# Kernel tuning notes

Measured on AMD Instinct MI355X. Metric: run time of the kernel, lower is better.

The kernel has to match this reference:

```python
import jax, jax.numpy as jnp
import numpy as np

B, S, D = 4, 4096, 64   # batch, seq_len, input_size
H, HD = 4, 16           # num_heads, head_dim


def setup_inputs() -> dict:
    key = jax.random.key(0)
    ks = jax.random.split(key, 9)
    sd = 1.0 / np.sqrt(D)          # torch Linear default uniform(-1/sqrt(fan_in), ...)
    so = 1.0 / np.sqrt(H * HD)
    u = lambda k, shape, s: jax.random.uniform(k, shape, jnp.float32, -s, s)
    return {
        "x": jax.random.normal(ks[0], (B, S, D), jnp.float32),
        "Wq": u(ks[1], (H, D, HD), sd), "bq": u(ks[2], (H, HD), sd),
        "Wk": u(ks[3], (H, D, HD), sd), "bk": u(ks[4], (H, HD), sd),
        "Wv": u(ks[5], (H, D, HD), sd), "bv": u(ks[6], (H, HD), sd),
        "Wo": u(ks[7], (H * HD, D), so), "bo": u(ks[8], (D,), so),
    }


def reference(x, Wq, bq, Wk, bk, Wv, bv, Wo, bo):
    # Batched per-head projections (fuses the original per-head Linear loop)
    q = jnp.einsum('bsd,hde->bhse', x, Wq) + bq[None, :, None, :]
    k = jnp.einsum('bsd,hde->bhse', x, Wk) + bk[None, :, None, :]
    v = jnp.einsum('bsd,hde->bhse', x, Wv) + bv[None, :, None, :]
    # scores: [B, H, S(query), S(key)]
    scores = jnp.einsum('bhse,bhte->bhst', q, k) / np.sqrt(HD).astype(np.float32)
    # FAITHFUL quirk: torch Softmax(dim=1) on [B,S,S] normalizes over the QUERY axis
    w = jax.nn.softmax(scores, axis=2)
    attended = jnp.einsum('bhst,bhte->bhse', w, v)          # [B,H,S,HD]
    concat = attended.transpose(0, 2, 1, 3).reshape(B, S, H * HD)
    out = concat @ Wo + bo                                   # [B,S,D]
    # FAITHFUL quirk: final softmax over the sequence axis (dim=1)
    return jax.nn.softmax(out, axis=1)
```

## Files before the change

kernel.cpp:

```cpp
#include <hip/hip_runtime.h>
#include <hip/hip_bf16.h>


#define BB 4
#define SS 4096
#define DD 64
#define HH 4
#define HDD 16

typedef unsigned int u32;
typedef unsigned short u16;
typedef __attribute__((ext_vector_type(8))) short bfrag;
typedef __attribute__((ext_vector_type(4))) float floatx4;
typedef __attribute__((ext_vector_type(16))) float floatx16;
typedef __attribute__((ext_vector_type(2))) u32 u32x2;
typedef __attribute__((ext_vector_type(4))) u32 u32x4;

#define LOG2E 1.4426950408889634074f
#define QSCALE (LOG2E * 0.25f)

__device__ __forceinline__ float fexp2(float x) {
#if __has_builtin(__builtin_amdgcn_exp2f)
  return __builtin_amdgcn_exp2f(x);
#else
  float r; asm("v_exp_f32 %0, %1" : "=v"(r) : "v"(x)); return r;
#endif
}
__device__ __forceinline__ float frcp(float x) {
#if __has_builtin(__builtin_amdgcn_rcpf)
  return __builtin_amdgcn_rcpf(x);
#else
  float r; asm("v_rcp_f32 %0, %1" : "=v"(r) : "v"(x)); return r;
#endif
}

__device__ __forceinline__ u16 f2bf(float f) {
  u32 u = __builtin_bit_cast(u32, f);
  return (u16)((u + 0x7FFFu + ((u >> 16) & 1u)) >> 16);
}
__device__ __forceinline__ u32 pack_bf(float lo, float hi) {
#if __has_builtin(__builtin_amdgcn_perm)
  return __builtin_amdgcn_perm(__builtin_bit_cast(u32, hi),
                               __builtin_bit_cast(u32, lo), 0x07060302u);
#else
  u32 a = __builtin_bit_cast(u32, lo);
  u32 b = __builtin_bit_cast(u32, hi);
  return (a >> 16) | (b & 0xFFFF0000u);
#endif
}

__device__ __forceinline__ void gload_lds16(const u16* g, u16* l) {
  __builtin_amdgcn_global_load_lds(
      (const __attribute__((address_space(1))) void*)(g),
      (__attribute__((address_space(3))) void*)(l), 16, 0, 0);
}

__device__ __forceinline__ int tmap(int c) {
  int c5 = c & 31;
  return (c & ~31) + (c5 & 3) + ((c5 >> 2) & 1) * 8 + ((c5 >> 3) & 1) * 16
       + ((c5 >> 4) & 1) * 4;
}

__global__ __launch_bounds__(256) void k_proj(
    const float* __restrict__ x,
    const float* __restrict__ Wq, const float* __restrict__ bq,
    const float* __restrict__ Wk, const float* __restrict__ bk,
    const float* __restrict__ Wv, const float* __restrict__ bv,
    u16* __restrict__ qb, u16* __restrict__ kb, float* __restrict__ vf)
{
  __shared__ float xs[16 * 64];
  const int tid = threadIdx.x;
  const int blk = blockIdx.x;
  const int b   = blk >> 8;
  const int s0  = (blk & 255) << 4;
  ((float4*)xs)[tid] = ((const float4*)(x + ((size_t)b * SS + s0) * DD))[tid];
  __syncthreads();

  const int col = tid & 63, h = col >> 4, e = col & 15;
  const int rg  = tid >> 6;
  float aq[4] = {0,0,0,0}, ak[4] = {0,0,0,0}, av[4] = {0,0,0,0};
  const int wofs = h * (DD * HDD) + e;
#pragma unroll 4
  for (int d = 0; d < DD; ++d) {
    float wq = Wq[wofs + d * HDD];
    float wk = Wk[wofs + d * HDD];
    float wv = Wv[wofs + d * HDD];
    const float* xr = xs + (rg * 4) * 64 + d;
#pragma unroll
    for (int r = 0; r < 4; ++r) {
      float xv = xr[r * 64];
      aq[r] += xv * wq; ak[r] += xv * wk; av[r] += xv * wv;
    }
  }
  const float bqv = bq[col], bkv = bk[col], bvv = bv[col];
  size_t base = ((size_t)(b * HH + h) * SS + (s0 + rg * 4)) * HDD + e;
#pragma unroll
  for (int r = 0; r < 4; ++r) {
    qb[base + r * HDD] = f2bf((aq[r] + bqv) * QSCALE);
    kb[base + r * HDD] = f2bf(ak[r] + bkv);
    vf[base + r * HDD] = av[r] + bvv;
  }
}

__global__ __launch_bounds__(512, 4) void k_csvp(
    const u16* __restrict__ qb, const u16* __restrict__ kb,
    const float* __restrict__ vf, u16* __restrict__ vp)
{
  __shared__ float vstage[128 * 16];
  __shared__ float cpart[2][128];
  __shared__ float rcl[128];
  const int tid = threadIdx.x;
  const int lane = tid & 63, w = tid >> 6;
  const int l31 = lane & 31, hl = lane >> 5;
  const int bx = blockIdx.x;
  const int bh = blockIdx.y;
  const int t0 = bx * 128 + (w & 3) * 32;
  const int shalf = w >> 2;
  const size_t base = (size_t)bh * (SS * HDD);

  {
    const float4* vsrc4 = (const float4*)(vf + ((size_t)bh * SS + bx * 128) * HDD);
    ((float4*)vstage)[tid] = vsrc4[tid];
  }

  const bfrag kf = *(const bfrag*)(kb + base + (size_t)(t0 + l31) * HDD + hl * 8);
  const u16* qpc = qb + base + ((size_t)shalf * 2048 + l31) * HDD + hl * 8;
  const floatx16 z16 = {0.f};
  float c0 = 0.f, c1 = 0.f, c2 = 0.f, c3 = 0.f;

#define LQ(i) (*(const bfrag*)(qpc + (size_t)(i) * (32 * HDD)))
#define ACCUM(dv)                                   \
  do {                                              \
    _Pragma("unroll")                               \
    for (int j = 0; j < 4; ++j) {                   \
      c0 += fexp2((dv)[4 * j + 0]);                 \
      c1 += fexp2((dv)[4 * j + 1]);                 \
      c2 += fexp2((dv)[4 * j + 2]);                 \
      c3 += fexp2((dv)[4 * j + 3]);                 \
    }                                               \
  } while (0)
#define STEP(qr, ri)                                                        \
  do {                                                                      \
    floatx16 dB = __builtin_amdgcn_mfma_f32_32x32x16_bf16(qr, kf, z16, 0, 0, 0); \
    qr = LQ(ri);                                                            \
    ACCUM(dA);                                                              \
    dA = dB;                                                                \
  } while (0)

  bfrag q0 = LQ(0), q1 = LQ(1), q2v = LQ(2), q3 = LQ(3);
  floatx16 dA = __builtin_amdgcn_mfma_f32_32x32x16_bf16(q0, kf, z16, 0, 0, 0);
  q0 = LQ(4);
#pragma unroll 1
  for (int o = 0; o < 2; ++o) {
#pragma unroll
    for (int i = 0; i < 32; i += 4) {
      STEP(q1,  i + 5);
      STEP(q2v, i + 6);
      STEP(q3,  i + 7);
      STEP(q0,  i + 8);
    }
    qpc += 32 * 32 * HDD;
  }
#undef STEP
#undef LQ
#undef ACCUM

  float c = (c0 + c1) + (c2 + c3);
  c += __shfl_xor(c, 32, 64);
  if (hl == 0)
    cpart[shalf][(w & 3) * 32 + l31] = c;
  __syncthreads();
  if (tid < 128)
    rcl[tid] = frcp(cpart[0][tid] + cpart[1][tid]);
  __syncthreads();

  if (tid < 256) {
    const int e = tid >> 4;
    const int h0 = bx & 1;
    const int poff = h0 * 16 + (tid & 15);
    const int cc = poff ^ (e & 7);
    const int h128 = h0 * 128;
    u32 r[4];
#pragma unroll
    for (int jj = 0; jj < 4; ++jj) {
      int ta = tmap(cc * 8 + 2 * jj)     - h128;
      int tb = tmap(cc * 8 + 2 * jj + 1) - h128;
      u16 lo = f2bf(vstage[ta * 16 + e] * rcl[ta]);
      u16 hi = f2bf(vstage[tb * 16 + e] * rcl[tb]);
      r[jj] = (u32)lo | ((u32)hi << 16);
    }
    u16* outb = vp + ((size_t)bh * 16 + (bx >> 1)) * 4096;
    u32x4 vv = {r[0], r[1], r[2], r[3]};
    *(u32x4*)(outb + e * 256 + poff * 8) = vv;
  }
}

__global__ __launch_bounds__(256, 4) void k_attn(
    const u16* __restrict__ qb, const u16* __restrict__ kb,
    const u16* __restrict__ vp, float* __restrict__ attp)
{
  __shared__ __align__(16) u16 vls[2][4096];
  const int tid  = threadIdx.x;
  const int lane = tid & 63, w = tid >> 6;
  const int l31 = lane & 31, hl = lane >> 5;
  const int bh = blockIdx.z, b = bh >> 2, h = bh & 3;
  const int tph = blockIdx.y;
  const int s0 = blockIdx.x * 128 + w * 32;
  const size_t base = (size_t)bh * (SS * HDD);

  const bfrag qf = *(const bfrag*)(qb + base + (size_t)(s0 + l31) * HDD + hl * 8);
  const u16* kp = kb + base + ((size_t)tph * 2048 + l31) * HDD + hl * 8;
  const floatx16 z16 = {0.f};
  floatx16 acc = {0.f};

  const u16* vsrc = vp + ((size_t)bh * 16 + tph * 8) * 4096;

  {
    const u16* gs = vsrc + w * 1024 + lane * 8;
    u16* ls = &vls[0][0] + w * 1024;
    gload_lds16(gs, ls);
    gload_lds16(gs + 512, ls + 512);
  }
  bfrag kfr[8];
#pragma unroll
  for (int it = 0; it < 8; ++it)
    kfr[it] = *(const bfrag*)(kp + (size_t)(it * 32) * HDD);
  floatx16 dA = __builtin_amdgcn_mfma_f32_32x32x16_bf16(kfr[0], qf, z16, 0, 0, 0);
  __syncthreads();

#pragma unroll
  for (int ch = 0; ch < 8; ++ch) {
    if (ch < 7) {
      const u16* gs = vsrc + (ch + 1) * 4096 + w * 1024 + lane * 8;
      u16* ls = &vls[(ch + 1) & 1][0] + w * 1024;
      gload_lds16(gs, ls);
      gload_lds16(gs + 512, ls + 512);
    }

    const u16* vrow = &vls[ch & 1][0] + (l31 & 15) * 256;
    const int eb = l31 & 7;
#pragma unroll
    for (int it = 0; it < 8; ++it) {
      if (ch < 7)
        kfr[it] = *(const bfrag*)(kp + (size_t)((ch + 1) * 256 + it * 32) * HDD);
      floatx16 dB;
      if (ch == 7 && it == 7) {
        dB = dA;
      } else {
        bfrag kn = (it < 7) ? kfr[it + 1] : kfr[0];
        dB = __builtin_amdgcn_mfma_f32_32x32x16_bf16(kn, qf, z16, 0, 0, 0);
      }
      u32 wr[8];
#pragma unroll
      for (int p = 0; p < 8; ++p)
        wr[p] = pack_bf(fexp2(dA[2 * p]), fexp2(dA[2 * p + 1]));
      const int cc0 = it * 4 + hl * 2;
      u32x4 af0 = *(const u32x4*)(vrow + ((cc0 ^ eb) << 3));
      u32x4 af1 = *(const u32x4*)(vrow + (((cc0 + 1) ^ eb) << 3));
      u32x4 ef0 = {wr[0], wr[1], wr[2], wr[3]};
      u32x4 ef1 = {wr[4], wr[5], wr[6], wr[7]};
      acc = __builtin_amdgcn_mfma_f32_32x32x16_bf16(
          __builtin_bit_cast(bfrag, af0), __builtin_bit_cast(bfrag, ef0), acc, 0, 0, 0);
      acc = __builtin_amdgcn_mfma_f32_32x32x16_bf16(
          __builtin_bit_cast(bfrag, af1), __builtin_bit_cast(bfrag, ef1), acc, 0, 0, 0);
      dA = dB;
    }
    __syncthreads();
  }

  float* ao = attp + (((size_t)tph * BB + b) * SS + s0 + l31) * (HH * HDD)
            + h * HDD + 4 * hl;
  float4 lo4 = {acc[0], acc[1], acc[2], acc[3]};
  float4 hi4 = {acc[4], acc[5], acc[6], acc[7]};
  *(float4*)ao       = lo4;
  *(float4*)(ao + 8) = hi4;
}

__global__ __launch_bounds__(256) void k_oproj(
    const float* __restrict__ att, const float* __restrict__ Wo,
    const float* __restrict__ bo, float* __restrict__ outp,
    float* __restrict__ part)
{
  __shared__ float wols[64 * 64];
  __shared__ float red[4][64];
  const int tid = threadIdx.x;
  const int blk = blockIdx.x;
  const int b = blk >> 9, s0 = (blk & 511) << 3;
#pragma unroll
  for (int i = 0; i < 4; ++i)
    ((float4*)wols)[tid + 256 * i] = ((const float4*)Wo)[tid + 256 * i];
  __syncthreads();

  const int d = tid & 63, sg = tid >> 6;
  const float bov = bo[d];
  const size_t so = (size_t)BB * SS * 16;
  float es = 0.f;
#pragma unroll
  for (int r = 0; r < 2; ++r) {
    int s = s0 + sg * 2 + r;
    const floatx4* row = (const floatx4*)(att + ((size_t)b * SS + s) * 64);
    float acc = bov;
#pragma unroll
    for (int j = 0; j < 16; ++j) {
      floatx4 c = row[j] + row[j + so];
      acc += c[0] * wols[(4*j+0)*64 + d] + c[1] * wols[(4*j+1)*64 + d]
           + c[2] * wols[(4*j+2)*64 + d] + c[3] * wols[(4*j+3)*64 + d];
    }
    outp[((size_t)b * SS + s) * 64 + d] = acc;
    es += fexp2(acc * LOG2E);
  }
  red[sg][d] = es;
  __syncthreads();
  if (tid < 64)
    part[((size_t)b * 512 + (blk & 511)) * 64 + tid] =
        red[0][tid] + red[1][tid] + red[2][tid] + red[3][tid];
}

__global__ __launch_bounds__(256) void k_softmax(
    const float* __restrict__ outp, const float* __restrict__ part,
    float* __restrict__ out)
{
  __shared__ float red[4][64];
  __shared__ float rs[64];
  const int tid = threadIdx.x, d = tid & 63, sg = tid >> 6;
  const int st = blockIdx.x;
  const int b = blockIdx.y;
  {
    float e = 0.f;
    const float* pp = part + ((size_t)b * 512 + sg * 128) * 64 + d;
#pragma unroll 8
    for (int c = 0; c < 128; ++c) e += pp[c * 64];
    red[sg][d] = e;
  }
  __syncthreads();
  if (tid < 64)
    rs[tid] = frcp(red[0][tid] + red[1][tid] + red[2][tid] + red[3][tid]);
  __syncthreads();
  const float r = rs[d];
  const size_t rowbase = ((size_t)b * SS + st * 64 + sg * 16) * 64 + d;
#pragma unroll 4
  for (int i = 0; i < 16; ++i)
    out[rowbase + i * 64] = fexp2(outp[rowbase + i * 64] * LOG2E) * r;
}

extern "C" void kernel_launch(void* const* d_in, const int* in_sizes, int n_in,
                              void* d_out, int out_size, void* d_ws, size_t ws_size,
                              hipStream_t stream) {
  const float* x  = (const float*)d_in[0];
  const float* Wq = (const float*)d_in[1];
  const float* bq = (const float*)d_in[2];
  const float* Wk = (const float*)d_in[3];
  const float* bk = (const float*)d_in[4];
  const float* Wv = (const float*)d_in[5];
  const float* bv = (const float*)d_in[6];
  const float* Wo = (const float*)d_in[7];
  const float* bo = (const float*)d_in[8];

  char* ws = (char*)d_ws;
  constexpr size_t QB_OFF  = 0;
  constexpr size_t KB_OFF  = (size_t)2  << 20;
  constexpr size_t VF_OFF  = (size_t)4  << 20;
  constexpr size_t VP_OFF  = (size_t)8  << 20;
  constexpr size_t ATT_OFF = (size_t)10 << 20;
  constexpr size_t OUT_OFF = (size_t)18 << 20;
  constexpr size_t PT_OFF  = (size_t)22 << 20;

  u16*   qb   = (u16*)  (ws + QB_OFF);
  u16*   kb   = (u16*)  (ws + KB_OFF);
  float* vf   = (float*)(ws + VF_OFF);
  u16*   vpb  = (u16*)  (ws + VP_OFF);
  float* attp = (float*)(ws + ATT_OFF);
  float* outp = (float*)(ws + OUT_OFF);
  float* part = (float*)(ws + PT_OFF);
  float* out  = (float*)d_out;

  hipLaunchKernelGGL(k_proj,    dim3(1024),       dim3(256), 0, stream,
                     x, Wq, bq, Wk, bk, Wv, bv, qb, kb, vf);
  hipLaunchKernelGGL(k_csvp,    dim3(32, 16),     dim3(512), 0, stream,
                     qb, kb, vf, vpb);
  hipLaunchKernelGGL(k_attn,    dim3(32, 2, 16),  dim3(256), 0, stream,
                     qb, kb, vpb, attp);
  hipLaunchKernelGGL(k_oproj,   dim3(2048),       dim3(256), 0, stream,
                     attp, Wo, bo, outp, part);
  hipLaunchKernelGGL(k_softmax, dim3(64, 4),      dim3(256), 0, stream, outp, part, out);
}
```

Baseline: 183.0 us.

## Store K in fragment layout and stage it through LDS with V in attention

The projection kernel now writes K in an MFMA-fragment-ordered layout, so each lane's 16-byte fragment is contiguous. The attention kernel stages K chunks into a double-buffered LDS region alongside V using direct global-to-LDS loads, replacing per-wave global K loads. This lets all four waves share one K fetch per block. It also splits the PV accumulator into two independent chains to shorten the MFMA dependency and replaces __syncthreads with an explicit vmcnt wait plus barrier. In exchange, LDS use per block doubles, which may limit occupancy, and every chunk now waits on all outstanding loads before compute.

```diff
diff --git a/kernel.cpp b/kernel.cpp
--- a/kernel.cpp
+++ b/kernel.cpp
@@ -66,7 +66,7 @@
     const float* __restrict__ Wq, const float* __restrict__ bq,
     const float* __restrict__ Wk, const float* __restrict__ bk,
     const float* __restrict__ Wv, const float* __restrict__ bv,
-    u16* __restrict__ qb, u16* __restrict__ kb, float* __restrict__ vf)
+    u16* __restrict__ qb, u16* __restrict__ kfl, float* __restrict__ vf)
 {
   __shared__ float xs[16 * 64];
   const int tid = threadIdx.x;
@@ -93,17 +93,21 @@
     }
   }
   const float bqv = bq[col], bkv = bk[col], bvv = bv[col];
-  size_t base = ((size_t)(b * HH + h) * SS + (s0 + rg * 4)) * HDD + e;
+  const int bh = b * HH + h;
+  size_t base = ((size_t)bh * SS + (s0 + rg * 4)) * HDD + e;
 #pragma unroll
   for (int r = 0; r < 4; ++r) {
+    int t = s0 + rg * 4 + r;
     qb[base + r * HDD] = f2bf((aq[r] + bqv) * QSCALE);
-    kb[base + r * HDD] = f2bf(ak[r] + bkv);
     vf[base + r * HDD] = av[r] + bvv;
+    size_t kidx = (((size_t)bh * 128 + (t >> 5)) * 64
+                 + (e >> 3) * 32 + (t & 31)) * 8 + (e & 7);
+    kfl[kidx] = f2bf(ak[r] + bkv);
   }
 }
 
 __global__ __launch_bounds__(512, 4) void k_csvp(
-    const u16* __restrict__ qb, const u16* __restrict__ kb,
+    const u16* __restrict__ qb, const u16* __restrict__ kfl,
     const float* __restrict__ vf, u16* __restrict__ vp)
 {
   __shared__ float vstage[128 * 16];
@@ -114,7 +118,6 @@
   const int l31 = lane & 31, hl = lane >> 5;
   const int bx = blockIdx.x;
   const int bh = blockIdx.y;
-  const int t0 = bx * 128 + (w & 3) * 32;
   const int shalf = w >> 2;
   const size_t base = (size_t)bh * (SS * HDD);
 
@@ -123,7 +126,8 @@
     ((float4*)vstage)[tid] = vsrc4[tid];
   }
 
-  const bfrag kf = *(const bfrag*)(kb + base + (size_t)(t0 + l31) * HDD + hl * 8);
+  const int g = bx * 4 + (w & 3);
+  const bfrag kf = *(const bfrag*)(kfl + (((size_t)bh * 128 + g) * 64 + lane) * 8);
   const u16* qpc = qb + base + ((size_t)shalf * 2048 + l31) * HDD + hl * 8;
   const floatx16 z16 = {0.f};
   float c0 = 0.f, c1 = 0.f, c2 = 0.f, c3 = 0.f;
@@ -196,10 +200,11 @@
 }
 
 __global__ __launch_bounds__(256, 4) void k_attn(
-    const u16* __restrict__ qb, const u16* __restrict__ kb,
+    const u16* __restrict__ qb, const u16* __restrict__ kfl,
     const u16* __restrict__ vp, float* __restrict__ attp)
 {
   __shared__ __align__(16) u16 vls[2][4096];
+  __shared__ __align__(16) u16 kls[2][4096];
   const int tid  = threadIdx.x;
   const int lane = tid & 63, w = tid >> 6;
   const int l31 = lane & 31, hl = lane >> 5;
@@ -209,47 +214,52 @@
   const size_t base = (size_t)bh * (SS * HDD);
 
   const bfrag qf = *(const bfrag*)(qb + base + (size_t)(s0 + l31) * HDD + hl * 8);
-  const u16* kp = kb + base + ((size_t)tph * 2048 + l31) * HDD + hl * 8;
   const floatx16 z16 = {0.f};
-  floatx16 acc = {0.f};
-
-  const u16* vsrc = vp + ((size_t)bh * 16 + tph * 8) * 4096;
-
-  {
-    const u16* gs = vsrc + w * 1024 + lane * 8;
-    u16* ls = &vls[0][0] + w * 1024;
-    gload_lds16(gs, ls);
-    gload_lds16(gs + 512, ls + 512);
-  }
-  bfrag kfr[8];
-#pragma unroll
-  for (int it = 0; it < 8; ++it)
-    kfr[it] = *(const bfrag*)(kp + (size_t)(it * 32) * HDD);
-  floatx16 dA = __builtin_amdgcn_mfma_f32_32x32x16_bf16(kfr[0], qf, z16, 0, 0, 0);
-  __syncthreads();
+  floatx16 acc0 = {0.f}, acc1 = {0.f};
+
+  const u16* vsrc = vp  + ((size_t)bh * 16  + tph * 8)  * 4096;
+  const u16* ksrc = kfl + ((size_t)bh * 128 + tph * 64) * 512;
+
+#define STAGE(ch, buf)                                                \
+  do {                                                                \
+    const u16* gv = vsrc + (ch) * 4096 + w * 1024 + lane * 8;         \
+    u16* lv = &vls[buf][0] + w * 1024;                                \
+    gload_lds16(gv, lv);                                              \
+    gload_lds16(gv + 512, lv + 512);                                  \
+    const u16* gk = ksrc + (ch) * 4096 + w * 1024 + lane * 8;         \
+    u16* lk = &kls[buf][0] + w * 1024;                                \
+    gload_lds16(gk, lk);                                              \
+    gload_lds16(gk + 512, lk + 512);                                  \
+  } while (0)
+
+  STAGE(0, 0);
 
 #pragma unroll
   for (int ch = 0; ch < 8; ++ch) {
-    if (ch < 7) {
-      const u16* gs = vsrc + (ch + 1) * 4096 + w * 1024 + lane * 8;
-      u16* ls = &vls[(ch + 1) & 1][0] + w * 1024;
-      gload_lds16(gs, ls);
-      gload_lds16(gs + 512, ls + 512);
-    }
+    asm volatile("s_waitcnt vmcnt(0)" ::: "memory");
+    __builtin_amdgcn_s_barrier();
+    __builtin_amdgcn_sched_barrier(0);
+    if (ch < 7) STAGE(ch + 1, (ch + 1) & 1);
 
     const u16* vrow = &vls[ch & 1][0] + (l31 & 15) * 256;
+    const u16* krow = &kls[ch & 1][0];
     const int eb = l31 & 7;
+
+    bfrag kfr[4];
+#pragma unroll
+    for (int it = 0; it < 4; ++it)
+      kfr[it] = *(const bfrag*)(krow + it * 512 + lane * 8);
+    floatx16 dA = __builtin_amdgcn_mfma_f32_32x32x16_bf16(kfr[0], qf, z16, 0, 0, 0);
+
 #pragma unroll
     for (int it = 0; it < 8; ++it) {
-      if (ch < 7)
-        kfr[it] = *(const bfrag*)(kp + (size_t)((ch + 1) * 256 + it * 32) * HDD);
+      if (it < 4)
+        kfr[it & 3] = *(const bfrag*)(krow + (it + 4) * 512 + lane * 8);
       floatx16 dB;
-      if (ch == 7 && it == 7) {
+      if (it < 7)
+        dB = __builtin_amdgcn_mfma_f32_32x32x16_bf16(kfr[(it + 1) & 3], qf, z16, 0, 0, 0);
+      else
         dB = dA;
-      } else {
-        bfrag kn = (it < 7) ? kfr[it + 1] : kfr[0];
-        dB = __builtin_amdgcn_mfma_f32_32x32x16_bf16(kn, qf, z16, 0, 0, 0);
-      }
       u32 wr[8];
 #pragma unroll
       for (int p = 0; p < 8; ++p)
@@ -259,15 +269,16 @@
       u32x4 af1 = *(const u32x4*)(vrow + (((cc0 + 1) ^ eb) << 3));
       u32x4 ef0 = {wr[0], wr[1], wr[2], wr[3]};
       u32x4 ef1 = {wr[4], wr[5], wr[6], wr[7]};
-      acc = __builtin_amdgcn_mfma_f32_32x32x16_bf16(
-          __builtin_bit_cast(bfrag, af0), __builtin_bit_cast(bfrag, ef0), acc, 0, 0, 0);
-      acc = __builtin_amdgcn_mfma_f32_32x32x16_bf16(
-          __builtin_bit_cast(bfrag, af1), __builtin_bit_cast(bfrag, ef1), acc, 0, 0, 0);
+      acc0 = __builtin_amdgcn_mfma_f32_32x32x16_bf16(
+          __builtin_bit_cast(bfrag, af0), __builtin_bit_cast(bfrag, ef0), acc0, 0, 0, 0);
+      acc1 = __builtin_amdgcn_mfma_f32_32x32x16_bf16(
+          __builtin_bit_cast(bfrag, af1), __builtin_bit_cast(bfrag, ef1), acc1, 0, 0, 0);
       dA = dB;
     }
-    __syncthreads();
-  }
-
+  }
+#undef STAGE
+
+  floatx16 acc = acc0 + acc1;
   float* ao = attp + (((size_t)tph * BB + b) * SS + s0 + l31) * (HH * HDD)
             + h * HDD + 4 * hl;
   float4 lo4 = {acc[0], acc[1], acc[2], acc[3]};
@@ -358,7 +369,7 @@
 
   char* ws = (char*)d_ws;
   constexpr size_t QB_OFF  = 0;
-  constexpr size_t KB_OFF  = (size_t)2  << 20;
+  constexpr size_t KF_OFF  = (size_t)2  << 20;
   constexpr size_t VF_OFF  = (size_t)4  << 20;
   constexpr size_t VP_OFF  = (size_t)8  << 20;
   constexpr size_t ATT_OFF = (size_t)10 << 20;
@@ -366,7 +377,7 @@
   constexpr size_t PT_OFF  = (size_t)22 << 20;
 
   u16*   qb   = (u16*)  (ws + QB_OFF);
-  u16*   kb   = (u16*)  (ws + KB_OFF);
+  u16*   kfl  = (u16*)  (ws + KF_OFF);
   float* vf   = (float*)(ws + VF_OFF);
   u16*   vpb  = (u16*)  (ws + VP_OFF);
   float* attp = (float*)(ws + ATT_OFF);
@@ -375,11 +386,11 @@
   float* out  = (float*)d_out;
 
   hipLaunchKernelGGL(k_proj,    dim3(1024),       dim3(256), 0, stream,
-                     x, Wq, bq, Wk, bk, Wv, bv, qb, kb, vf);
+                     x, Wq, bq, Wk, bk, Wv, bv, qb, kfl, vf);
   hipLaunchKernelGGL(k_csvp,    dim3(32, 16),     dim3(512), 0, stream,
-                     qb, kb, vf, vpb);
+                     qb, kfl, vf, vpb);
   hipLaunchKernelGGL(k_attn,    dim3(32, 2, 16),  dim3(256), 0, stream,
-                     qb, kb, vpb, attp);
+                     qb, kfl, vpb, attp);
   hipLaunchKernelGGL(k_oproj,   dim3(2048),       dim3(256), 0, stream,
                      attp, Wo, bo, outp, part);
   hipLaunchKernelGGL(k_softmax, dim3(64, 4),      dim3(256), 0, stream, outp, part, out);
```

New measurement: 179.6 us. About the same (-1.9%).
